# Performance work log

Hardware: AMD Instinct MI355X
Metric: run time of the kernel (lower is better)

The kernel has to match this reference:

```python
import jax, jax.numpy as jnp
import numpy as np

MARGIN = 0.5
N = 512
D = 2048
NUM_IDS = 64


def setup_inputs() -> dict:
    key = jax.random.key(0)
    k1, k2 = jax.random.split(key)
    inputs = jax.random.normal(k1, (N, D), dtype=jnp.float32)
    targets = jax.random.randint(k2, (N,), 0, NUM_IDS, dtype=jnp.int64)
    return {"inputs": inputs, "targets": targets}


def _pairwise_dist(x):
    # ||xi||^2 + ||xj||^2 - 2 xi.xj, clamped at 0, then sqrt (safe at 0)
    sq = jnp.sum(x * x, axis=1)
    d2 = sq[:, None] + sq[None, :] - 2.0 * (x @ x.T)
    d2 = jnp.clip(d2, 0.0)
    nz = d2 > 0
    return jnp.where(nz, jnp.sqrt(jnp.where(nz, d2, 1.0)), 0.0)


def reference(inputs, targets):
    n = inputs.shape[0]
    dist = _pairwise_dist(inputs)  # [n, n]
    same = targets[:, None] == targets[None, :]
    eye = jnp.eye(n, dtype=bool)
    pos = same & ~eye   # (i, j): valid positive pairs
    neg = ~same         # (i, k): valid negative pairs

    d_ap = dist[:, :, None]  # d[i, j] broadcast over k -> [n, n, 1]
    d_an = dist[:, None, :]  # d[i, k] broadcast over j -> [n, 1, n]

    # triplet (i, j, k) selected iff pos(i,j) & neg(i,k) & d_an - d_ap < margin
    viol = pos[:, :, None] & neg[:, None, :] & ((d_an - d_ap) < MARGIN)  # [n,n,n]

    # MarginRankingLoss(dist_an, dist_ap, y=1) = mean(max(0, dist_ap - dist_an + margin))
    per = jnp.maximum(d_ap - d_an + MARGIN, 0.0)
    cnt = jnp.sum(viol)
    total = jnp.sum(jnp.where(viol, per, 0.0))
    return total / jnp.maximum(cnt, 1).astype(per.dtype)
```

## Files before the change

### kernel.cpp

```cpp
#include <hip/hip_runtime.h>
#include <math.h>

#define NPTS 512
#define DIM  2048
#define MARGIN_F 0.5f
#define KZ 8
#define KCHUNK (DIM / KZ)

typedef __attribute__((ext_vector_type(4))) float f32x4;
typedef __attribute__((ext_vector_type(8))) short bf16x8;

__device__ inline unsigned short bfr(float f) {
    unsigned int u = __float_as_uint(f);
    u += 0x7FFFu + ((u >> 16) & 1u);
    return (unsigned short)(u >> 16);
}

__global__ __launch_bounds__(256) void gram_kernel(const float* __restrict__ x,
                                                   float* __restrict__ part,
                                                   float* __restrict__ diag) {
    __shared__ unsigned short As[64][72];
    __shared__ unsigned short Bs[64][72];

    int bx = blockIdx.x, by = blockIdx.y, z = blockIdx.z;
    int tid = threadIdx.x;
    int lr = tid >> 2;
    int lc = (tid & 3) * 16;

    const float* arow = x + (size_t)(bx * 64 + lr) * DIM + (size_t)z * KCHUNK + lc;
    const float* brow = x + (size_t)(by * 64 + lr) * DIM + (size_t)z * KCHUNK + lc;

    int w = tid >> 6, lane = tid & 63;
    int wr = (w >> 1) * 32, wc = (w & 1) * 32;
    int fr = lane & 15, ko = (lane >> 4) * 8;

    f32x4 acc[2][2] = {};

    for (int ks = 0; ks < KCHUNK; ks += 64) {
        float4 a0 = *reinterpret_cast<const float4*>(arow + ks);
        float4 a1 = *reinterpret_cast<const float4*>(arow + ks + 4);
        float4 a2 = *reinterpret_cast<const float4*>(arow + ks + 8);
        float4 a3 = *reinterpret_cast<const float4*>(arow + ks + 12);
        float4 b0 = *reinterpret_cast<const float4*>(brow + ks);
        float4 b1 = *reinterpret_cast<const float4*>(brow + ks + 4);
        float4 b2 = *reinterpret_cast<const float4*>(brow + ks + 8);
        float4 b3 = *reinterpret_cast<const float4*>(brow + ks + 12);
        ushort4 ua0 = { bfr(a0.x), bfr(a0.y), bfr(a0.z), bfr(a0.w) };
        ushort4 ua1 = { bfr(a1.x), bfr(a1.y), bfr(a1.z), bfr(a1.w) };
        ushort4 ua2 = { bfr(a2.x), bfr(a2.y), bfr(a2.z), bfr(a2.w) };
        ushort4 ua3 = { bfr(a3.x), bfr(a3.y), bfr(a3.z), bfr(a3.w) };
        ushort4 ub0 = { bfr(b0.x), bfr(b0.y), bfr(b0.z), bfr(b0.w) };
        ushort4 ub1 = { bfr(b1.x), bfr(b1.y), bfr(b1.z), bfr(b1.w) };
        ushort4 ub2 = { bfr(b2.x), bfr(b2.y), bfr(b2.z), bfr(b2.w) };
        ushort4 ub3 = { bfr(b3.x), bfr(b3.y), bfr(b3.z), bfr(b3.w) };
        *reinterpret_cast<ushort4*>(&As[lr][lc])      = ua0;
        *reinterpret_cast<ushort4*>(&As[lr][lc + 4])  = ua1;
        *reinterpret_cast<ushort4*>(&As[lr][lc + 8])  = ua2;
        *reinterpret_cast<ushort4*>(&As[lr][lc + 12]) = ua3;
        *reinterpret_cast<ushort4*>(&Bs[lr][lc])      = ub0;
        *reinterpret_cast<ushort4*>(&Bs[lr][lc + 4])  = ub1;
        *reinterpret_cast<ushort4*>(&Bs[lr][lc + 8])  = ub2;
        *reinterpret_cast<ushort4*>(&Bs[lr][lc + 12]) = ub3;
        __syncthreads();
#pragma unroll
        for (int kc = 0; kc < 2; ++kc) {
            bf16x8 fa0 = *reinterpret_cast<const bf16x8*>(&As[wr + fr][kc * 32 + ko]);
            bf16x8 fa1 = *reinterpret_cast<const bf16x8*>(&As[wr + 16 + fr][kc * 32 + ko]);
            bf16x8 fb0 = *reinterpret_cast<const bf16x8*>(&Bs[wc + fr][kc * 32 + ko]);
            bf16x8 fb1 = *reinterpret_cast<const bf16x8*>(&Bs[wc + 16 + fr][kc * 32 + ko]);
            acc[0][0] = __builtin_amdgcn_mfma_f32_16x16x32_bf16(fa0, fb0, acc[0][0], 0, 0, 0);
            acc[0][1] = __builtin_amdgcn_mfma_f32_16x16x32_bf16(fa0, fb1, acc[0][1], 0, 0, 0);
            acc[1][0] = __builtin_amdgcn_mfma_f32_16x16x32_bf16(fa1, fb0, acc[1][0], 0, 0, 0);
            acc[1][1] = __builtin_amdgcn_mfma_f32_16x16x32_bf16(fa1, fb1, acc[1][1], 0, 0, 0);
        }
        __syncthreads();
    }

    float* pg = part + (size_t)z * NPTS * NPTS;
    int rbase = bx * 64 + wr + ((lane >> 4) << 2);
    int cbase = by * 64 + wc + fr;
#pragma unroll
    for (int m = 0; m < 2; ++m)
#pragma unroll
        for (int n = 0; n < 2; ++n) {
            f32x4 v = acc[m][n];
#pragma unroll
            for (int j = 0; j < 4; ++j)
                pg[(size_t)(rbase + m * 16 + j) * NPTS + (cbase + n * 16)] = v[j];
        }

    if (bx == by && wr == wc && (fr >> 2) == (lane >> 4)) {
        int j = fr & 3;
#pragma unroll
        for (int m = 0; m < 2; ++m)
            diag[(size_t)z * NPTS + bx * 64 + wr + m * 16 + fr] = acc[m][m][j];
    }
}

__global__ __launch_bounds__(256) void triplet_kernel(const float* __restrict__ part,
                                                      const float* __restrict__ diag,
                                                      const int* __restrict__ traw,
                                                      float* __restrict__ psum,
                                                      unsigned int* __restrict__ pcnt) {
    __shared__ float drow[NPTS];
    __shared__ float sqv[NPTS];
    __shared__ int   tl[NPTS];
    __shared__ int   pos[NPTS];
    __shared__ int   is64;
    __shared__ unsigned long long wmask[8];
    __shared__ float wsum[4];
    __shared__ unsigned int wcnt[4];

    int a = blockIdx.x, tid = threadIdx.x;
    int lane = tid & 63, wid = tid >> 6;
    if (tid == 0) is64 = 1;
    __syncthreads();

    for (int i = tid; i < NPTS / 2; i += 256)
        if (traw[2 * i + 1] != 0) is64 = 0;
    __syncthreads();
    if (is64) { for (int i = tid; i < NPTS; i += 256) tl[i] = traw[2 * i]; }
    else      { for (int i = tid; i < NPTS; i += 256) tl[i] = traw[i]; }

    for (int j = tid; j < NPTS; j += 256) {
        float s = 0.f;
#pragma unroll
        for (int z = 0; z < KZ; ++z) s += diag[(size_t)z * NPTS + j];
        sqv[j] = s;
    }
    __syncthreads();

    const size_t PL = (size_t)NPTS * NPTS;
    float sqa = sqv[a];
    for (int i = tid; i < NPTS / 4; i += 256) {
        float4 g4 = {0.f, 0.f, 0.f, 0.f};
#pragma unroll
        for (int z = 0; z < KZ; ++z) {
            float4 gz = reinterpret_cast<const float4*>(part + (size_t)z * PL + (size_t)a * NPTS)[i];
            g4.x += gz.x; g4.y += gz.y; g4.z += gz.z; g4.w += gz.w;
        }
        float d2;
        d2 = sqa + sqv[4 * i + 0] - 2.f * g4.x; drow[4 * i + 0] = d2 > 0.f ? sqrtf(d2) : 0.f;
        d2 = sqa + sqv[4 * i + 1] - 2.f * g4.y; drow[4 * i + 1] = d2 > 0.f ? sqrtf(d2) : 0.f;
        d2 = sqa + sqv[4 * i + 2] - 2.f * g4.z; drow[4 * i + 2] = d2 > 0.f ? sqrtf(d2) : 0.f;
        d2 = sqa + sqv[4 * i + 3] - 2.f * g4.w; drow[4 * i + 3] = d2 > 0.f ? sqrtf(d2) : 0.f;
    }
    __syncthreads();

    int ta = tl[a];
    unsigned long long bal[2];
    bool m[2];
#pragma unroll
    for (int p = 0; p < 2; ++p) {
        int j = p * 256 + tid;
        m[p] = (tl[j] == ta) && (j != a);
        bal[p] = __ballot(m[p]);
        if (lane == 0) wmask[p * 4 + wid] = bal[p];
    }
    __syncthreads();
    int np = 0;
#pragma unroll
    for (int k = 0; k < 8; ++k) np += __popcll(wmask[k]);
#pragma unroll
    for (int p = 0; p < 2; ++p) {
        if (m[p]) {
            int widx = p * 4 + wid, base = 0;
            for (int k = 0; k < widx; ++k) base += __popcll(wmask[k]);
            base += __popcll(bal[p] & ((1ull << lane) - 1ull));
            pos[base] = p * 256 + tid;
        }
    }
    __syncthreads();

    float sum = 0.f;
    unsigned int cnt = 0;
    int tot = np << 9;
    for (int idx = tid; idx < tot; idx += 256) {
        int p = pos[idx >> 9];
        int n = idx & (NPTS - 1);
        if (tl[n] != ta) {
            float v = drow[p] - drow[n] + MARGIN_F;
            if (v > 0.f) { sum += v; cnt++; }
        }
    }

    for (int off = 32; off; off >>= 1) {
        sum += __shfl_down(sum, off);
        cnt += __shfl_down(cnt, off);
    }
    if (lane == 0) { wsum[wid] = sum; wcnt[wid] = cnt; }
    __syncthreads();
    if (tid == 0) {
        psum[a] = wsum[0] + wsum[1] + wsum[2] + wsum[3];
        pcnt[a] = wcnt[0] + wcnt[1] + wcnt[2] + wcnt[3];
    }
}

__global__ __launch_bounds__(256) void finalize_kernel(const float* __restrict__ psum,
                                                       const unsigned int* __restrict__ pcnt,
                                                       float* __restrict__ out) {
    int tid = threadIdx.x;
    float s = psum[tid] + psum[tid + 256];
    unsigned int c = pcnt[tid] + pcnt[tid + 256];
    for (int off = 32; off; off >>= 1) {
        s += __shfl_down(s, off);
        c += __shfl_down(c, off);
    }
    __shared__ float ws[4];
    __shared__ unsigned int wc[4];
    int lane = tid & 63, wid = tid >> 6;
    if (lane == 0) { ws[wid] = s; wc[wid] = c; }
    __syncthreads();
    if (tid == 0) {
        float tot = ws[0] + ws[1] + ws[2] + ws[3];
        unsigned int cnt = wc[0] + wc[1] + wc[2] + wc[3];
        out[0] = tot / (float)(cnt ? cnt : 1u);
    }
}

extern "C" void kernel_launch(void* const* d_in, const int* in_sizes, int n_in,
                              void* d_out, int out_size, void* d_ws, size_t ws_size,
                              hipStream_t stream) {
    const float* x = (const float*)d_in[0];
    const int* t = (const int*)d_in[1];
    float* out = (float*)d_out;

    char* ws = (char*)d_ws;
    const size_t OFF_PART = 0;
    const size_t OFF_DIAG = (size_t)KZ * NPTS * NPTS * 4;
    const size_t OFF_PSUM = OFF_DIAG + (size_t)KZ * NPTS * 4;
    const size_t OFF_PCNT = OFF_PSUM + 2048;

    float* part        = (float*)(ws + OFF_PART);
    float* diag        = (float*)(ws + OFF_DIAG);
    float* psum        = (float*)(ws + OFF_PSUM);
    unsigned int* pcnt = (unsigned int*)(ws + OFF_PCNT);

    gram_kernel<<<dim3(8, 8, KZ), 256, 0, stream>>>(x, part, diag);
    triplet_kernel<<<NPTS, 256, 0, stream>>>(part, diag, t, psum, pcnt);
    finalize_kernel<<<1, 256, 0, stream>>>(psum, pcnt, out);
}
```

Before: 24.98 us.

## Fuse finalize into triplet kernel via last-block ticket and pack bf16 conversions

Drops the separate finalize kernel launch. Each triplet block now takes an atomic ticket on a counter that the gram kernel resets, and the last block to finish does the final reduction. The gram kernel now converts to bf16 with the native __bf16 cast, packs two values per 32-bit word, and writes to LDS with 128-bit stores instead of 64-bit ones. The distance-row loop is rewritten as a single float2 pass per thread. This saves one launch and some conversion work, at the cost of an atomic plus fences in every triplet block.

```diff
diff --git a/kernel.cpp b/kernel.cpp
--- a/kernel.cpp
+++ b/kernel.cpp
@@ -9,21 +9,26 @@
 
 typedef __attribute__((ext_vector_type(4))) float f32x4;
 typedef __attribute__((ext_vector_type(8))) short bf16x8;
-
-__device__ inline unsigned short bfr(float f) {
-    unsigned int u = __float_as_uint(f);
-    u += 0x7FFFu + ((u >> 16) & 1u);
-    return (unsigned short)(u >> 16);
+typedef __attribute__((ext_vector_type(4))) unsigned int u32x4;
+
+__device__ inline unsigned int pkbf(float lo, float hi) {
+    unsigned short ul = __builtin_bit_cast(unsigned short, (__bf16)lo);
+    unsigned short uh = __builtin_bit_cast(unsigned short, (__bf16)hi);
+    return (unsigned int)ul | ((unsigned int)uh << 16);
 }
 
 __global__ __launch_bounds__(256) void gram_kernel(const float* __restrict__ x,
                                                    float* __restrict__ part,
-                                                   float* __restrict__ diag) {
-    __shared__ unsigned short As[64][72];
-    __shared__ unsigned short Bs[64][72];
+                                                   float* __restrict__ diag,
+                                                   unsigned int* __restrict__ ctr) {
+    __shared__ __align__(16) unsigned short As[64][72];
+    __shared__ __align__(16) unsigned short Bs[64][72];
 
     int bx = blockIdx.x, by = blockIdx.y, z = blockIdx.z;
     int tid = threadIdx.x;
+
+    if (bx == 0 && by == 0 && z == 0 && tid == 0) ctr[0] = 0u;
+
     int lr = tid >> 2;
     int lc = (tid & 3) * 16;
 
@@ -45,22 +50,14 @@
         float4 b1 = *reinterpret_cast<const float4*>(brow + ks + 4);
         float4 b2 = *reinterpret_cast<const float4*>(brow + ks + 8);
         float4 b3 = *reinterpret_cast<const float4*>(brow + ks + 12);
-        ushort4 ua0 = { bfr(a0.x), bfr(a0.y), bfr(a0.z), bfr(a0.w) };
-        ushort4 ua1 = { bfr(a1.x), bfr(a1.y), bfr(a1.z), bfr(a1.w) };
-        ushort4 ua2 = { bfr(a2.x), bfr(a2.y), bfr(a2.z), bfr(a2.w) };
-        ushort4 ua3 = { bfr(a3.x), bfr(a3.y), bfr(a3.z), bfr(a3.w) };
-        ushort4 ub0 = { bfr(b0.x), bfr(b0.y), bfr(b0.z), bfr(b0.w) };
-        ushort4 ub1 = { bfr(b1.x), bfr(b1.y), bfr(b1.z), bfr(b1.w) };
-        ushort4 ub2 = { bfr(b2.x), bfr(b2.y), bfr(b2.z), bfr(b2.w) };
-        ushort4 ub3 = { bfr(b3.x), bfr(b3.y), bfr(b3.z), bfr(b3.w) };
-        *reinterpret_cast<ushort4*>(&As[lr][lc])      = ua0;
-        *reinterpret_cast<ushort4*>(&As[lr][lc + 4])  = ua1;
-        *reinterpret_cast<ushort4*>(&As[lr][lc + 8])  = ua2;
-        *reinterpret_cast<ushort4*>(&As[lr][lc + 12]) = ua3;
-        *reinterpret_cast<ushort4*>(&Bs[lr][lc])      = ub0;
-        *reinterpret_cast<ushort4*>(&Bs[lr][lc + 4])  = ub1;
-        *reinterpret_cast<ushort4*>(&Bs[lr][lc + 8])  = ub2;
-        *reinterpret_cast<ushort4*>(&Bs[lr][lc + 12]) = ub3;
+        u32x4 wa0 = { pkbf(a0.x, a0.y), pkbf(a0.z, a0.w), pkbf(a1.x, a1.y), pkbf(a1.z, a1.w) };
+        u32x4 wa1 = { pkbf(a2.x, a2.y), pkbf(a2.z, a2.w), pkbf(a3.x, a3.y), pkbf(a3.z, a3.w) };
+        u32x4 wb0 = { pkbf(b0.x, b0.y), pkbf(b0.z, b0.w), pkbf(b1.x, b1.y), pkbf(b1.z, b1.w) };
+        u32x4 wb1 = { pkbf(b2.x, b2.y), pkbf(b2.z, b2.w), pkbf(b3.x, b3.y), pkbf(b3.z, b3.w) };
+        *reinterpret_cast<u32x4*>(&As[lr][lc])     = wa0;
+        *reinterpret_cast<u32x4*>(&As[lr][lc + 8]) = wa1;
+        *reinterpret_cast<u32x4*>(&Bs[lr][lc])     = wb0;
+        *reinterpret_cast<u32x4*>(&Bs[lr][lc + 8]) = wb1;
         __syncthreads();
 #pragma unroll
         for (int kc = 0; kc < 2; ++kc) {
@@ -101,7 +98,9 @@
                                                       const float* __restrict__ diag,
                                                       const int* __restrict__ traw,
                                                       float* __restrict__ psum,
-                                                      unsigned int* __restrict__ pcnt) {
+                                                      unsigned int* __restrict__ pcnt,
+                                                      unsigned int* __restrict__ ctr,
+                                                      float* __restrict__ out) {
     __shared__ float drow[NPTS];
     __shared__ float sqv[NPTS];
     __shared__ int   tl[NPTS];
@@ -110,6 +109,7 @@
     __shared__ unsigned long long wmask[8];
     __shared__ float wsum[4];
     __shared__ unsigned int wcnt[4];
+    __shared__ unsigned int ticket_s;
 
     int a = blockIdx.x, tid = threadIdx.x;
     int lane = tid & 63, wid = tid >> 6;
@@ -132,18 +132,17 @@
 
     const size_t PL = (size_t)NPTS * NPTS;
     float sqa = sqv[a];
-    for (int i = tid; i < NPTS / 4; i += 256) {
-        float4 g4 = {0.f, 0.f, 0.f, 0.f};
+    {
+        int i = tid;
+        float2 g2 = {0.f, 0.f};
 #pragma unroll
         for (int z = 0; z < KZ; ++z) {
-            float4 gz = reinterpret_cast<const float4*>(part + (size_t)z * PL + (size_t)a * NPTS)[i];
-            g4.x += gz.x; g4.y += gz.y; g4.z += gz.z; g4.w += gz.w;
+            float2 gz = reinterpret_cast<const float2*>(part + (size_t)z * PL + (size_t)a * NPTS)[i];
+            g2.x += gz.x; g2.y += gz.y;
         }
         float d2;
-        d2 = sqa + sqv[4 * i + 0] - 2.f * g4.x; drow[4 * i + 0] = d2 > 0.f ? sqrtf(d2) : 0.f;
-        d2 = sqa + sqv[4 * i + 1] - 2.f * g4.y; drow[4 * i + 1] = d2 > 0.f ? sqrtf(d2) : 0.f;
-        d2 = sqa + sqv[4 * i + 2] - 2.f * g4.z; drow[4 * i + 2] = d2 > 0.f ? sqrtf(d2) : 0.f;
-        d2 = sqa + sqv[4 * i + 3] - 2.f * g4.w; drow[4 * i + 3] = d2 > 0.f ? sqrtf(d2) : 0.f;
+        d2 = sqa + sqv[2 * i + 0] - 2.f * g2.x; drow[2 * i + 0] = d2 > 0.f ? sqrtf(d2) : 0.f;
+        d2 = sqa + sqv[2 * i + 1] - 2.f * g2.y; drow[2 * i + 1] = d2 > 0.f ? sqrtf(d2) : 0.f;
     }
     __syncthreads();
 
@@ -190,31 +189,29 @@
     }
     if (lane == 0) { wsum[wid] = sum; wcnt[wid] = cnt; }
     __syncthreads();
+
     if (tid == 0) {
         psum[a] = wsum[0] + wsum[1] + wsum[2] + wsum[3];
         pcnt[a] = wcnt[0] + wcnt[1] + wcnt[2] + wcnt[3];
-    }
-}
-
-__global__ __launch_bounds__(256) void finalize_kernel(const float* __restrict__ psum,
-                                                       const unsigned int* __restrict__ pcnt,
-                                                       float* __restrict__ out) {
-    int tid = threadIdx.x;
-    float s = psum[tid] + psum[tid + 256];
-    unsigned int c = pcnt[tid] + pcnt[tid + 256];
-    for (int off = 32; off; off >>= 1) {
-        s += __shfl_down(s, off);
-        c += __shfl_down(c, off);
-    }
-    __shared__ float ws[4];
-    __shared__ unsigned int wc[4];
-    int lane = tid & 63, wid = tid >> 6;
-    if (lane == 0) { ws[wid] = s; wc[wid] = c; }
-    __syncthreads();
-    if (tid == 0) {
-        float tot = ws[0] + ws[1] + ws[2] + ws[3];
-        unsigned int cnt = wc[0] + wc[1] + wc[2] + wc[3];
-        out[0] = tot / (float)(cnt ? cnt : 1u);
+        __threadfence();
+        ticket_s = atomicAdd(ctr, 1u);
+    }
+    __syncthreads();
+    if (ticket_s == NPTS - 1) {
+        __threadfence();
+        float s = psum[tid] + psum[tid + 256];
+        unsigned int c = pcnt[tid] + pcnt[tid + 256];
+        for (int off = 32; off; off >>= 1) {
+            s += __shfl_down(s, off);
+            c += __shfl_down(c, off);
+        }
+        if (lane == 0) { wsum[wid] = s; wcnt[wid] = c; }
+        __syncthreads();
+        if (tid == 0) {
+            float totv = wsum[0] + wsum[1] + wsum[2] + wsum[3];
+            unsigned int cc = wcnt[0] + wcnt[1] + wcnt[2] + wcnt[3];
+            out[0] = totv / (float)(cc ? cc : 1u);
+        }
     }
 }
 
@@ -230,13 +227,14 @@
     const size_t OFF_DIAG = (size_t)KZ * NPTS * NPTS * 4;
     const size_t OFF_PSUM = OFF_DIAG + (size_t)KZ * NPTS * 4;
     const size_t OFF_PCNT = OFF_PSUM + 2048;
+    const size_t OFF_CTR  = OFF_PCNT + 2048;
 
     float* part        = (float*)(ws + OFF_PART);
     float* diag        = (float*)(ws + OFF_DIAG);
     float* psum        = (float*)(ws + OFF_PSUM);
     unsigned int* pcnt = (unsigned int*)(ws + OFF_PCNT);
-
-    gram_kernel<<<dim3(8, 8, KZ), 256, 0, stream>>>(x, part, diag);
-    triplet_kernel<<<NPTS, 256, 0, stream>>>(part, diag, t, psum, pcnt);
-    finalize_kernel<<<1, 256, 0, stream>>>(psum, pcnt, out);
-}
+    unsigned int* ctr  = (unsigned int*)(ws + OFF_CTR);
+
+    gram_kernel<<<dim3(8, 8, KZ), 256, 0, stream>>>(x, part, diag, ctr);
+    triplet_kernel<<<NPTS, 256, 0, stream>>>(part, diag, t, psum, pcnt, ctr, out);
+}
```

Measured after the change: 31.35 us. +25.5%, slower.
